# Kernel optimization log

Measured on AMD Instinct MI355X. Metric: run time of the kernel, lower is better.

The kernel has to match this reference:

```python
import jax, jax.numpy as jnp
import numpy as np

TRUNC = 2.0  # NSFP truncated chamfer: squared dists >= 2 are zeroed


def _mlp(x, W0, b0, Wh, bh, Wl, bl):
    h = jax.nn.relu(x @ W0 + b0)
    for i in range(Wh.shape[0]):
        h = jax.nn.relu(h @ Wh[i] + bh[i])
    return h @ Wl + bl


def _chamfer(x, y):
    d = (jnp.sum(x * x, axis=1)[:, None]
         + jnp.sum(y * y, axis=1)[None, :]
         - 2.0 * (x @ y.T))
    dx = jnp.min(d, axis=1)  # [N] NN dist x->y
    dy = jnp.min(d, axis=0)  # [M] NN dist y->x
    dx = jnp.where(dx < TRUNC, dx, 0.0)
    dy = jnp.where(dy < TRUNC, dy, 0.0)
    return jnp.mean(dx) + jnp.mean(dy)


def setup_inputs() -> dict:
    key = jax.random.key(0)
    ks = jax.random.split(key, 16)
    N = 20000
    F = 128
    H = 7  # hidden 128->128 layers (layer_size=8)
    s_in = 1.0 / np.sqrt(3.0)
    s_h = 1.0 / np.sqrt(F)
    d = {
        'pc0': jax.random.normal(ks[0], (N, 3), jnp.float32) * 10.0,
        'pc1': jax.random.normal(ks[1], (N, 3), jnp.float32) * 10.0,
        'W0': jax.random.normal(ks[2], (3, F), jnp.float32) * s_in,
        'b0': jnp.zeros((F,), jnp.float32),
        'Wh': jax.random.normal(ks[3], (H, F, F), jnp.float32) * s_h,
        'bh': jnp.zeros((H, F), jnp.float32),
        'Wl': jax.random.normal(ks[4], (F, 3), jnp.float32) * s_h,
        'bl': jnp.zeros((3,), jnp.float32),
        'W0i': jax.random.normal(ks[5], (3, F), jnp.float32) * s_in,
        'b0i': jnp.zeros((F,), jnp.float32),
        'Whi': jax.random.normal(ks[6], (H, F, F), jnp.float32) * s_h,
        'bhi': jnp.zeros((H, F), jnp.float32),
        'Wli': jax.random.normal(ks[7], (F, 3), jnp.float32) * s_h,
        'bli': jnp.zeros((3,), jnp.float32),
    }
    return d


def reference(pc0, pc1, W0, b0, Wh, bh, Wl, bl,
              W0i, b0i, Whi, bhi, Wli, bli):
    forward_flow = _mlp(pc0, W0, b0, Wh, bh, Wl, bl)          # [N,3]
    pc0_to_pc1 = pc0 + forward_flow
    inverse_flow = _mlp(pc0_to_pc1, W0i, b0i, Whi, bhi, Wli, bli)
    est_pc1_to_pc0 = pc0_to_pc1 - inverse_flow
    forward_loss = _chamfer(pc0_to_pc1, pc1)
    inverse_loss = _chamfer(est_pc1_to_pc0, pc0)
    return forward_loss + inverse_loss


if __name__ == '__main__':
    out = reference(**setup_inputs())
    print(out)
```

## Files before the change

### kernel.cpp

```cpp
#include <hip/hip_runtime.h>
#include <hip/hip_bf16.h>

#define F 128
#define NHID 7
#define BP 80
#define NPT 5
#define TRUNC_ 2.0f

#define GM 32
#define GM3 (GM * GM * GM)
#define GLO (-28.0f)
#define CELL 1.75f
#define GINV (1.0f / 1.75f)
#define SCAN_BLKS (GM3 / 256)
#define NGRID 4
#define PACKB 112
#define ZCB 128
#define ZB (NGRID * GM3 / 256)
#define BQ 128

typedef __attribute__((ext_vector_type(8))) short short8v;
typedef __attribute__((ext_vector_type(4))) float f32x4;

__device__ inline unsigned short f2bf(float v)
{
    __hip_bfloat16 b = __float2bfloat16(v);
    return __builtin_bit_cast(unsigned short, b);
}
__device__ inline float bf2f(unsigned short u)
{
    unsigned int x = ((unsigned int)u) << 16;
    return __builtin_bit_cast(float, x);
}

__device__ inline int hsw(int row, int col)
{
    return row * 128 + ((((col >> 3) ^ (row & 7)) << 3) | (col & 7));
}

__device__ inline void barrier_nd()
{
    asm volatile("s_waitcnt lgkmcnt(0)" ::: "memory");
    __builtin_amdgcn_s_barrier();
}

__global__ __launch_bounds__(256) void prep_kernel(
    const float* __restrict__ Wh, const float* __restrict__ Whi,
    const float* __restrict__ Wl, const float* __restrict__ Wli,
    unsigned short* __restrict__ whp,
    float* __restrict__ wlt, int* __restrict__ counts, unsigned int* __restrict__ done)
{
    int bid = blockIdx.x;
    int t = threadIdx.x;
    if (bid < PACKB) {
        int g = bid * 256 + t;
        int l = g & 63;
        int tt = (g >> 6) & 7;
        int s = (g >> 9) & 3;
        int m = g >> 11;
        int k0 = s * 32 + (l >> 4) * 8;
        int c = tt * 16 + (l & 15);
        const float* W = (m < 7 ? Wh + (size_t)m * F * F
                                : Whi + (size_t)(m - 7) * F * F);
        short8v v;
#pragma unroll
        for (int j = 0; j < 8; ++j)
            v[j] = (short)f2bf(W[(k0 + j) * F + c]);
        *(short8v*)(whp + (size_t)g * 8) = v;
    } else if (bid < PACKB + ZCB) {
        *(int4*)&counts[((bid - PACKB) * 256 + t) * 4] = make_int4(0, 0, 0, 0);
    } else {
#pragma unroll
        for (int r = 0; r < 3; ++r) {
            int e = r * 256 + t;
            int mI = e / 384;
            int rem = e - mI * 384;
            int c = rem >> 7;
            int k = rem & 127;
            const float* W = mI ? Wli : Wl;
            wlt[e] = W[k * 3 + c];
        }
        if (t == 0) *done = 0u;
    }
}

__device__ inline int cell_of(float x, float y, float z)
{
    int cx = (int)floorf((x - GLO) * GINV);
    int cy = (int)floorf((y - GLO) * GINV);
    int cz = (int)floorf((z - GLO) * GINV);
    cx = min(max(cx, 0), GM - 1);
    cy = min(max(cy, 0), GM - 1);
    cz = min(max(cz, 0), GM - 1);
    return (cz * GM + cy) * GM + cx;
}

__global__ __launch_bounds__(512, 2) void mlp_fused_kernel(
    const float* __restrict__ pc0, const float* __restrict__ pc1,
    const float* __restrict__ W0a, const float* __restrict__ b0a,
    const float* __restrict__ W0b, const float* __restrict__ b0b,
    const unsigned short* __restrict__ whp,
    const float* __restrict__ bha, const float* __restrict__ bhb,
    const float* __restrict__ wlt,
    const float* __restrict__ bla, const float* __restrict__ blb,
    float* __restrict__ Aout, float* __restrict__ Cout,
    int* __restrict__ counts, int N)
{
    __shared__ unsigned short hX[BP * 128];
    __shared__ unsigned short hY[BP * 128];
    __shared__ float Al[BP][4];
    __shared__ float Cl[BP][4];

    const int tid = threadIdx.x;
    const int lane = tid & 63;
    const int wv = tid >> 6;
    const int arow = lane & 15;
    const int kg = lane >> 4;
    const int p0 = blockIdx.x * BP;

    unsigned short* cur = hX;
    unsigned short* nxt = hY;

    short8v wA, wB;
    short8v hA[NPT], hB[NPT];

#define LW(WD, LI, S) { \
        size_t off = ((size_t)(((LI) * 4 + (S)) * 8 + wv) * 64 + lane) * 8; \
        WD = *(const short8v*)(whp + off); }
#define LH(D, S) { _Pragma("unroll") for (int p = 0; p < NPT; ++p) \
        D[p] = *(const short8v*)&cur[hsw(p * 16 + arow, (S) * 32 + kg * 8)]; }
#define MM(WD, H) { \
    _Pragma("unroll") for (int p = 0; p < NPT; ++p) \
        acc[p] = __builtin_amdgcn_mfma_f32_16x16x32_bf16(WD, H[p], acc[p], 0, 0, 0); }

    LW(wA, 0, 0)
    LW(wB, 0, 1)
    __builtin_amdgcn_sched_barrier(0);

    for (int M = 0; M < 2; ++M) {
        const float* W0 = M ? W0b : W0a;
        const float* b0 = M ? b0b : b0a;
        const float* bh = M ? bhb : bha;
        const float* bl = M ? blb : bla;

        {
            const int jg = tid & 31;
            const int pgg = tid >> 5;
            const int j0 = jg * 4;
            float4 wr0 = *(const float4*)(W0 + 0 * F + j0);
            float4 wr1 = *(const float4*)(W0 + 1 * F + j0);
            float4 wr2 = *(const float4*)(W0 + 2 * F + j0);
            float4 bb0 = *(const float4*)(b0 + j0);
#pragma unroll
            for (int p = 0; p < 5; ++p) {
                int pt = pgg * 5 + p;
                float x0, x1, x2;
                if (M == 0) {
                    int gp = p0 + pt;
                    int cp = gp < N ? gp : N - 1;
                    x0 = pc0[cp * 3 + 0]; x1 = pc0[cp * 3 + 1]; x2 = pc0[cp * 3 + 2];
                } else {
                    x0 = Al[pt][0]; x1 = Al[pt][1]; x2 = Al[pt][2];
                }
                float hx = fmaxf(fmaf(x0, wr0.x, fmaf(x1, wr1.x, fmaf(x2, wr2.x, bb0.x))), 0.f);
                float hy = fmaxf(fmaf(x0, wr0.y, fmaf(x1, wr1.y, fmaf(x2, wr2.y, bb0.y))), 0.f);
                float hz = fmaxf(fmaf(x0, wr0.z, fmaf(x1, wr1.z, fmaf(x2, wr2.z, bb0.z))), 0.f);
                float hw = fmaxf(fmaf(x0, wr0.w, fmaf(x1, wr1.w, fmaf(x2, wr2.w, bb0.w))), 0.f);
                short4 hv = make_short4((short)f2bf(hx), (short)f2bf(hy),
                                        (short)f2bf(hz), (short)f2bf(hw));
                *(short4*)&cur[hsw(pt, j0)] = hv;
            }
        }
        barrier_nd();

        for (int l = 0; l < NHID; ++l) {
            const int L = M * 7 + l;
            const int Ln = (L + 1 < 14) ? (L + 1) : 13;
            f32x4 acc[NPT];
            {
                float4 b4 = *(const float4*)&bh[l * F + wv * 16 + kg * 4];
#pragma unroll
                for (int p = 0; p < NPT; ++p)
                    acc[p] = (f32x4){b4.x, b4.y, b4.z, b4.w};
            }

            LH(hA, 0) LH(hB, 1)
            __builtin_amdgcn_sched_barrier(0);
            MM(wA, hA)
            LW(wA, L, 2) LH(hA, 2)
            __builtin_amdgcn_sched_barrier(0);
            MM(wB, hB)
            LW(wB, L, 3) LH(hB, 3)
            __builtin_amdgcn_sched_barrier(0);
            MM(wA, hA)
            LW(wA, Ln, 0)
            __builtin_amdgcn_sched_barrier(0);
            MM(wB, hB)
            LW(wB, Ln, 1)

#pragma unroll
            for (int p = 0; p < NPT; ++p) {
                float v0 = fmaxf(acc[p][0], 0.f), v1 = fmaxf(acc[p][1], 0.f);
                float v2 = fmaxf(acc[p][2], 0.f), v3 = fmaxf(acc[p][3], 0.f);
                short4 hv = make_short4((short)f2bf(v0), (short)f2bf(v1),
                                        (short)f2bf(v2), (short)f2bf(v3));
                *(short4*)&nxt[hsw(p * 16 + arow, wv * 16 + kg * 4)] = hv;
            }
            barrier_nd();
            unsigned short* tsw = cur; cur = nxt; nxt = tsw;
        }

        if (tid < 240) {
            int pt = tid / 3;
            int c = tid - 3 * pt;
            const float* wl = wlt + M * 384 + c * 128;
            float a0 = 0.f, a1 = 0.f, a2 = 0.f, a3 = 0.f;
#pragma unroll
            for (int q = 0; q < 16; ++q) {
                short8v h8 = *(const short8v*)&cur[hsw(pt, q * 8)];
                float4 wa = *(const float4*)(wl + q * 8);
                float4 wb = *(const float4*)(wl + q * 8 + 4);
                a0 = fmaf(bf2f((unsigned short)h8[0]), wa.x, a0);
                a1 = fmaf(bf2f((unsigned short)h8[1]), wa.y, a1);
                a2 = fmaf(bf2f((unsigned short)h8[2]), wa.z, a2);
                a3 = fmaf(bf2f((unsigned short)h8[3]), wa.w, a3);
                a0 = fmaf(bf2f((unsigned short)h8[4]), wb.x, a0);
                a1 = fmaf(bf2f((unsigned short)h8[5]), wb.y, a1);
                a2 = fmaf(bf2f((unsigned short)h8[6]), wb.z, a2);
                a3 = fmaf(bf2f((unsigned short)h8[7]), wb.w, a3);
            }
            float flow = ((a0 + a1) + (a2 + a3)) + bl[c];
            int gp = p0 + pt;
            int cp = gp < N ? gp : N - 1;
            if (M == 0) {
                float val = pc0[cp * 3 + c] + flow;
                Al[pt][c] = val;
                if (gp < N) Aout[gp * 3 + c] = val;
            } else {
                float val = Al[pt][c] - flow;
                Cl[pt][c] = val;
                if (gp < N) Cout[gp * 3 + c] = val;
            }
        }
        barrier_nd();
    }
#undef LW
#undef LH
#undef MM

    if (tid < BP) {
        int gp = p0 + tid;
        if (gp < N) {
            atomicAdd(&counts[1 * GM3 + cell_of(Al[tid][0], Al[tid][1], Al[tid][2])], 1);
            atomicAdd(&counts[3 * GM3 + cell_of(Cl[tid][0], Cl[tid][1], Cl[tid][2])], 1);
            atomicAdd(&counts[0 * GM3 + cell_of(pc1[gp * 3 + 0], pc1[gp * 3 + 1], pc1[gp * 3 + 2])], 1);
            atomicAdd(&counts[2 * GM3 + cell_of(pc0[gp * 3 + 0], pc0[gp * 3 + 1], pc0[gp * 3 + 2])], 1);
        }
    }
}

__device__ inline const float* cloud_ptr(int g, const float* g0, const float* g1,
                                         const float* g2, const float* g3)
{
    return g == 0 ? g0 : (g == 1 ? g1 : (g == 2 ? g2 : g3));
}

__global__ __launch_bounds__(256) void scan1(
    const int* __restrict__ counts, int* __restrict__ offs, int* __restrict__ bsum)
{
    int tid = threadIdx.x;
    int i = blockIdx.x * 256 + tid;
    int v = counts[i];
    __shared__ int s[256];
    s[tid] = v;
    __syncthreads();
#pragma unroll
    for (int off = 1; off < 256; off <<= 1) {
        int t = (tid >= off) ? s[tid - off] : 0;
        __syncthreads();
        s[tid] += t;
        __syncthreads();
    }
    offs[i] = s[tid] - v;
    if (tid == 255) bsum[blockIdx.x] = s[255];
}

__global__ __launch_bounds__(256) void scan23(
    int* __restrict__ offs, const int* __restrict__ bsum, int* __restrict__ counts)
{
    int seg = blockIdx.x / SCAN_BLKS;
    int pos = blockIdx.x - seg * SCAN_BLKS;
    const int* bs = bsum + seg * SCAN_BLKS;
    int t = threadIdx.x;
    int v = (t < pos) ? bs[t] : 0;
    __shared__ int red[4];
#pragma unroll
    for (int o = 32; o > 0; o >>= 1) v += __shfl_down(v, o, 64);
    if ((t & 63) == 0) red[t >> 6] = v;
    __syncthreads();
    int prefix = red[0] + red[1] + red[2] + red[3];
    int i = blockIdx.x * 256 + t;
    offs[i] += prefix;
    counts[i] = 0;
}

__global__ __launch_bounds__(256) void grid_fill(
    const float* __restrict__ B, const float* __restrict__ A,
    const float* __restrict__ D, const float* __restrict__ C,
    const int* __restrict__ offs, int* __restrict__ counts,
    float4* __restrict__ pts, int n)
{
    int g = blockIdx.y;
    const float* P = cloud_ptr(g, B, A, D, C);
    int i = blockIdx.x * 256 + threadIdx.x;
    if (i < n) {
        float x = P[i * 3 + 0], y = P[i * 3 + 1], z = P[i * 3 + 2];
        int c = g * GM3 + cell_of(x, y, z);
        int slot = offs[c] + atomicAdd(&counts[c], 1);
        pts[(size_t)g * n + slot] = make_float4(x, y, z, 0.f);
    }
}

__device__ inline float block_sum256(float v)
{
    __shared__ float sws[4];
#pragma unroll
    for (int o = 32; o > 0; o >>= 1) v += __shfl_down(v, o, 64);
    int w = threadIdx.x >> 6;
    if ((threadIdx.x & 63) == 0) sws[w] = v;
    __syncthreads();
    if (threadIdx.x == 0) v = sws[0] + sws[1] + sws[2] + sws[3];
    return v;
}

__device__ inline float boxd1(float q, int c)
{
    float lo = GLO + c * CELL;
    return fmaxf(fmaxf(lo - q, q - (lo + CELL)), 0.f);
}

__global__ __launch_bounds__(256) void grid_search(
    const int* __restrict__ offs, const int* __restrict__ counts,
    const float4* __restrict__ pts, float* __restrict__ partials,
    unsigned int* __restrict__ done, float* __restrict__ out, float inv, int n)
{
    const int d = blockIdx.y;
    const float4* Qs = pts + (size_t)(d ^ 1) * n;
    const float4* P  = pts + (size_t)d * n;
    const int* ofs = offs + (size_t)d * GM3;
    const int* cnt = counts + (size_t)d * GM3;

    const int tid = threadIdx.x;
    const int ql = tid & (BQ - 1);
    const int half = tid >> 7;
    const int i = blockIdx.x * BQ + ql;

    float mn = 3.4e38f;
    if (i < n) {
        float4 q = Qs[i];
        int cx = min(max((int)floorf((q.x - GLO) * GINV), 0), GM - 1);
        int cy = min(max((int)floorf((q.y - GLO) * GINV), 0), GM - 1);
        int cz = min(max((int)floorf((q.z - GLO) * GINV), 0), GM - 1);
        int xcl = max(cx - 1, 0), xch = min(cx + 1, GM - 1);
        int r0 = half * 4;

        int o[5], e[5];
#pragma unroll
        for (int r = 0; r < 5; ++r) {
            o[r] = 0; e[r] = 0;
            bool act = half ? true : (r < 4);
            if (act) {
                int rr = r0 + r;
                int dz = rr / 3, dy = rr - dz * 3;
                int z = cz + dz - 1;
                int y = cy + dy - 1;
                if ((unsigned)z < GM && (unsigned)y < GM) {
                    float dzd = boxd1(q.z, z);
                    float dyd = boxd1(q.y, y);
                    float dyz2 = fmaf(dzd, dzd, dyd * dyd);
                    if (dyz2 < TRUNC_) {
                        float rx = sqrtf(TRUNC_ - dyz2);
                        int xlo = max((int)floorf((q.x - rx - GLO) * GINV), xcl);
                        int xhi = min((int)floorf((q.x + rx - GLO) * GINV), xch);
                        if (xlo <= xhi) {
                            int rowbase = (z * GM + y) * GM;
                            o[r] = ofs[rowbase + xlo];
                            e[r] = ofs[rowbase + xhi] + cnt[rowbase + xhi];
                        }
                    }
                }
            }
        }
#pragma unroll
        for (int r = 0; r < 5; ++r) {
            for (int k = o[r]; k < e[r]; ++k) {
                float4 p = P[k];
                float ddx = q.x - p.x, ddy = q.y - p.y, ddz = q.z - p.z;
                mn = fminf(mn, fmaf(ddx, ddx, fmaf(ddy, ddy, ddz * ddz)));
            }
        }
    }

    __shared__ float m0[BQ];
    if (half == 0) m0[ql] = mn;
    __syncthreads();
    float val = 0.f;
    if (half == 1 && i < n) {
        float m = fminf(mn, m0[ql]);
        val = (m < TRUNC_) ? m : 0.f;
    }
    float bs = block_sum256(val);

    __shared__ int lastflag;
    if (tid == 0) {
        atomicExch(&partials[(size_t)d * gridDim.x + blockIdx.x], bs);
        __threadfence();
        unsigned v = atomicAdd(done, 1u);
        lastflag = (v == (unsigned)(NGRID * gridDim.x - 1)) ? 1 : 0;
    }
    __syncthreads();
    if (lastflag) {
        int NPt = NGRID * gridDim.x;
        float s = 0.f;
        for (int j = tid; j < NPt; j += 256)
            s += atomicAdd(&partials[j], 0.0f);
        __syncthreads();
        float tot = block_sum256(s);
        if (tid == 0) out[0] = tot * inv;
    }
}

extern "C" void kernel_launch(void* const* d_in, const int* in_sizes, int n_in,
                              void* d_out, int out_size, void* d_ws, size_t ws_size,
                              hipStream_t stream)
{
    const float* pc0 = (const float*)d_in[0];
    const float* pc1 = (const float*)d_in[1];
    const float* W0  = (const float*)d_in[2];
    const float* b0  = (const float*)d_in[3];
    const float* Wh  = (const float*)d_in[4];
    const float* bh  = (const float*)d_in[5];
    const float* Wl  = (const float*)d_in[6];
    const float* bl  = (const float*)d_in[7];
    const float* W0i = (const float*)d_in[8];
    const float* b0i = (const float*)d_in[9];
    const float* Whi = (const float*)d_in[10];
    const float* bhi = (const float*)d_in[11];
    const float* Wli = (const float*)d_in[12];
    const float* bli = (const float*)d_in[13];
    float* out = (float*)d_out;

    const int N = in_sizes[0] / 3;

    char* base = (char*)d_ws;
    float*  A        = (float*)(base + 0);
    float*  C        = (float*)(base + 240000);
    int*    counts   = (int*)  (base + 480000);
    int*    offs     = (int*)  (base + 1004288);
    int*    bsum     = (int*)  (base + 1528576);
    float4* pts      = (float4*)(base + 1532672);
    float*  partials = (float*)(base + 2812672);
    unsigned int* done = (unsigned int*)(base + 2816768);
    unsigned short* whp = (unsigned short*)(base + 2816784);
    float*  wlt      = (float*)(base + 3275536);

    const int PB = (N + 255) / 256;
    const int QB = (N + BQ - 1) / BQ;

    hipLaunchKernelGGL(prep_kernel, dim3(PACKB + ZCB + 1), dim3(256), 0, stream,
                       Wh, Whi, Wl, Wli, whp, wlt, counts, done);

    int mlpg = (N + BP - 1) / BP;
    hipLaunchKernelGGL(mlp_fused_kernel, dim3(mlpg), dim3(512), 0, stream,
                       pc0, pc1, W0, b0, W0i, b0i, whp, bh, bhi,
                       wlt, bl, bli, A, C, counts, N);

    hipLaunchKernelGGL(scan1, dim3(ZB), dim3(256), 0, stream, counts, offs, bsum);
    hipLaunchKernelGGL(scan23, dim3(ZB), dim3(256), 0, stream, offs, bsum, counts);
    hipLaunchKernelGGL(grid_fill, dim3(PB, NGRID), dim3(256), 0, stream,
                       pc1, A, pc0, C, offs, counts, pts, N);

    hipLaunchKernelGGL(grid_search, dim3(QB, NGRID), dim3(256), 0, stream,
                       offs, counts, pts, partials, done, out,
                       1.0f / (float)N, N);
}
```

Before: 76.67 us.

## Split MLP MFMA work across waves by point and feature groups

Each of the 8 waves previously owned 16 output features for all 80 points, so it loaded one weight fragment and all five point tiles from LDS per k-step. Now waves form a 2x4 grid: two point groups (3 or 2 tiles) by four feature groups (32 features each). Each wave loads two weight fragments and fewer LDS activation tiles, which cuts LDS reads. The cost is more weight loads per wave from global memory or cache, plus an uneven 3/2 point split that leaves some waves with less work.

```diff
diff --git a/kernel.cpp b/kernel.cpp
--- a/kernel.cpp
+++ b/kernel.cpp
@@ -4,7 +4,6 @@
 #define F 128
 #define NHID 7
 #define BP 80
-#define NPT 5
 #define TRUNC_ 2.0f
 
 #define GM 32
@@ -114,6 +113,10 @@
     const int tid = threadIdx.x;
     const int lane = tid & 63;
     const int wv = tid >> 6;
+    const int pg = wv & 1;
+    const int fg = wv >> 1;
+    const int pbase = pg * 3;
+    const int npt = pg ? 2 : 3;
     const int arow = lane & 15;
     const int kg = lane >> 4;
     const int p0 = blockIdx.x * BP;
@@ -121,20 +124,22 @@
     unsigned short* cur = hX;
     unsigned short* nxt = hY;
 
-    short8v wA, wB;
-    short8v hA[NPT], hB[NPT];
-
-#define LW(WD, LI, S) { \
-        size_t off = ((size_t)(((LI) * 4 + (S)) * 8 + wv) * 64 + lane) * 8; \
-        WD = *(const short8v*)(whp + off); }
-#define LH(D, S) { _Pragma("unroll") for (int p = 0; p < NPT; ++p) \
-        D[p] = *(const short8v*)&cur[hsw(p * 16 + arow, (S) * 32 + kg * 8)]; }
-#define MM(WD, H) { \
-    _Pragma("unroll") for (int p = 0; p < NPT; ++p) \
-        acc[p] = __builtin_amdgcn_mfma_f32_16x16x32_bf16(WD, H[p], acc[p], 0, 0, 0); }
-
-    LW(wA, 0, 0)
-    LW(wB, 0, 1)
+    short8v wA0, wA1, wB0, wB1;
+    short8v hA[3], hB[3];
+
+#define LW(WD0, WD1, LI, S) { \
+        size_t off = ((size_t)(((LI) * 4 + (S)) * 8 + fg * 2) * 64 + lane) * 8; \
+        WD0 = *(const short8v*)(whp + off); \
+        WD1 = *(const short8v*)(whp + off + 512); }
+#define LH(D, S) { _Pragma("unroll") for (int p = 0; p < 3; ++p) if (p < npt) \
+        D[p] = *(const short8v*)&cur[hsw((pbase + p) * 16 + arow, (S) * 32 + kg * 8)]; }
+#define MM(WD0, WD1, H) { \
+    _Pragma("unroll") for (int p = 0; p < 3; ++p) if (p < npt) { \
+        acc[p][0] = __builtin_amdgcn_mfma_f32_16x16x32_bf16(WD0, H[p], acc[p][0], 0, 0, 0); \
+        acc[p][1] = __builtin_amdgcn_mfma_f32_16x16x32_bf16(WD1, H[p], acc[p][1], 0, 0, 0); } }
+
+    LW(wA0, wA1, 0, 0)
+    LW(wB0, wB1, 0, 1)
     __builtin_amdgcn_sched_barrier(0);
 
     for (int M = 0; M < 2; ++M) {
@@ -176,35 +181,43 @@
         for (int l = 0; l < NHID; ++l) {
             const int L = M * 7 + l;
             const int Ln = (L + 1 < 14) ? (L + 1) : 13;
-            f32x4 acc[NPT];
-            {
-                float4 b4 = *(const float4*)&bh[l * F + wv * 16 + kg * 4];
-#pragma unroll
-                for (int p = 0; p < NPT; ++p)
-                    acc[p] = (f32x4){b4.x, b4.y, b4.z, b4.w};
+            f32x4 acc[3][2];
+#pragma unroll
+            for (int p = 0; p < 3; ++p) {
+#pragma unroll
+                for (int m = 0; m < 2; ++m) {
+                    float4 b4 = *(const float4*)&bh[l * F + (fg * 2 + m) * 16 + kg * 4];
+                    acc[p][m] = (f32x4){b4.x, b4.y, b4.z, b4.w};
+                }
             }
 
             LH(hA, 0) LH(hB, 1)
             __builtin_amdgcn_sched_barrier(0);
-            MM(wA, hA)
-            LW(wA, L, 2) LH(hA, 2)
+            MM(wA0, wA1, hA)
+            LW(wA0, wA1, L, 2) LH(hA, 2)
             __builtin_amdgcn_sched_barrier(0);
-            MM(wB, hB)
-            LW(wB, L, 3) LH(hB, 3)
+            MM(wB0, wB1, hB)
+            LW(wB0, wB1, L, 3) LH(hB, 3)
             __builtin_amdgcn_sched_barrier(0);
-            MM(wA, hA)
-            LW(wA, Ln, 0)
+            MM(wA0, wA1, hA)
+            LW(wA0, wA1, Ln, 0)
             __builtin_amdgcn_sched_barrier(0);
-            MM(wB, hB)
-            LW(wB, Ln, 1)
-
-#pragma unroll
-            for (int p = 0; p < NPT; ++p) {
-                float v0 = fmaxf(acc[p][0], 0.f), v1 = fmaxf(acc[p][1], 0.f);
-                float v2 = fmaxf(acc[p][2], 0.f), v3 = fmaxf(acc[p][3], 0.f);
-                short4 hv = make_short4((short)f2bf(v0), (short)f2bf(v1),
-                                        (short)f2bf(v2), (short)f2bf(v3));
-                *(short4*)&nxt[hsw(p * 16 + arow, wv * 16 + kg * 4)] = hv;
+            MM(wB0, wB1, hB)
+            LW(wB0, wB1, Ln, 1)
+
+#pragma unroll
+            for (int p = 0; p < 3; ++p) {
+                if (p < npt) {
+#pragma unroll
+                    for (int m = 0; m < 2; ++m) {
+                        float v0 = fmaxf(acc[p][m][0], 0.f), v1 = fmaxf(acc[p][m][1], 0.f);
+                        float v2 = fmaxf(acc[p][m][2], 0.f), v3 = fmaxf(acc[p][m][3], 0.f);
+                        short4 hv = make_short4((short)f2bf(v0), (short)f2bf(v1),
+                                                (short)f2bf(v2), (short)f2bf(v3));
+                        *(short4*)&nxt[hsw((pbase + p) * 16 + arow,
+                                           (fg * 2 + m) * 16 + kg * 4)] = hv;
+                    }
+                }
             }
             barrier_nd();
             unsigned short* tsw = cur; cur = nxt; nxt = tsw;
```

New measurement: 78.19 us. About the same (+2.0%).

## Compute both chamfer directions from one search pass using atomicMin on targets

Applied to the files above, without the earlier changes.

Grid search now runs over two directions instead of four. Each query-to-target distance below the truncation is also pushed into a per-target atomicMin buffer, which supplies the reverse nearest-neighbour distance. The buffer is initialised in the prep kernel, and the last block sums it serially in the final reduction. This halves the neighbour search work, but adds many global atomics in the inner loop and a serial 2N-element reduction in a single block.

```diff
diff --git a/kernel.cpp b/kernel.cpp
--- a/kernel.cpp
+++ b/kernel.cpp
@@ -14,8 +14,10 @@
 #define GINV (1.0f / 1.75f)
 #define SCAN_BLKS (GM3 / 256)
 #define NGRID 4
+#define NDIR 2
 #define PACKB 112
 #define ZCB 128
+#define QMB 40
 #define ZB (NGRID * GM3 / 256)
 #define BQ 128
 
@@ -48,7 +50,8 @@
     const float* __restrict__ Wh, const float* __restrict__ Whi,
     const float* __restrict__ Wl, const float* __restrict__ Wli,
     unsigned short* __restrict__ whp,
-    float* __restrict__ wlt, int* __restrict__ counts, unsigned int* __restrict__ done)
+    float* __restrict__ wlt, int* __restrict__ counts,
+    unsigned int* __restrict__ done, unsigned int* __restrict__ qmins)
 {
     int bid = blockIdx.x;
     int t = threadIdx.x;
@@ -69,7 +72,7 @@
         *(short8v*)(whp + (size_t)g * 8) = v;
     } else if (bid < PACKB + ZCB) {
         *(int4*)&counts[((bid - PACKB) * 256 + t) * 4] = make_int4(0, 0, 0, 0);
-    } else {
+    } else if (bid == PACKB + ZCB) {
 #pragma unroll
         for (int r = 0; r < 3; ++r) {
             int e = r * 256 + t;
@@ -81,6 +84,10 @@
             wlt[e] = W[k * 3 + c];
         }
         if (t == 0) *done = 0u;
+    } else {
+        const unsigned int inf = 0x7f7fffffu;
+        uint4 v = make_uint4(inf, inf, inf, inf);
+        *(uint4*)&qmins[((bid - PACKB - ZCB - 1) * 256 + t) * 4] = v;
     }
 }
 
@@ -342,13 +349,16 @@
 __global__ __launch_bounds__(256) void grid_search(
     const int* __restrict__ offs, const int* __restrict__ counts,
     const float4* __restrict__ pts, float* __restrict__ partials,
+    unsigned int* __restrict__ qmins,
     unsigned int* __restrict__ done, float* __restrict__ out, float inv, int n)
 {
     const int d = blockIdx.y;
-    const float4* Qs = pts + (size_t)(d ^ 1) * n;
-    const float4* P  = pts + (size_t)d * n;
-    const int* ofs = offs + (size_t)d * GM3;
-    const int* cnt = counts + (size_t)d * GM3;
+    const int gq = 2 * d + 1, gt = 2 * d;
+    const float4* Qs = pts + (size_t)gq * n;
+    const float4* P  = pts + (size_t)gt * n;
+    const int* ofs = offs + (size_t)gt * GM3;
+    const int* cnt = counts + (size_t)gt * GM3;
+    unsigned int* qm = qmins + (size_t)d * n;
 
     const int tid = threadIdx.x;
     const int ql = tid & (BQ - 1);
@@ -396,7 +406,10 @@
             for (int k = o[r]; k < e[r]; ++k) {
                 float4 p = P[k];
                 float ddx = q.x - p.x, ddy = q.y - p.y, ddz = q.z - p.z;
-                mn = fminf(mn, fmaf(ddx, ddx, fmaf(ddy, ddy, ddz * ddz)));
+                float dd = fmaf(ddx, ddx, fmaf(ddy, ddy, ddz * ddz));
+                mn = fminf(mn, dd);
+                if (dd < TRUNC_)
+                    atomicMin(&qm[k], __float_as_uint(dd));
             }
         }
     }
@@ -416,14 +429,19 @@
         atomicExch(&partials[(size_t)d * gridDim.x + blockIdx.x], bs);
         __threadfence();
         unsigned v = atomicAdd(done, 1u);
-        lastflag = (v == (unsigned)(NGRID * gridDim.x - 1)) ? 1 : 0;
+        lastflag = (v == (unsigned)(NDIR * gridDim.x - 1)) ? 1 : 0;
     }
     __syncthreads();
     if (lastflag) {
-        int NPt = NGRID * gridDim.x;
+        int NPt = NDIR * gridDim.x;
         float s = 0.f;
         for (int j = tid; j < NPt; j += 256)
             s += atomicAdd(&partials[j], 0.0f);
+        for (int j = tid; j < 2 * n; j += 256) {
+            unsigned u = atomicAdd(&qmins[j], 0u);
+            float m = __uint_as_float(u);
+            s += (m < TRUNC_) ? m : 0.f;
+        }
         __syncthreads();
         float tot = block_sum256(s);
         if (tid == 0) out[0] = tot * inv;
@@ -463,12 +481,13 @@
     unsigned int* done = (unsigned int*)(base + 2816768);
     unsigned short* whp = (unsigned short*)(base + 2816784);
     float*  wlt      = (float*)(base + 3275536);
+    unsigned int* qmins = (unsigned int*)(base + 3278608);
 
     const int PB = (N + 255) / 256;
     const int QB = (N + BQ - 1) / BQ;
 
-    hipLaunchKernelGGL(prep_kernel, dim3(PACKB + ZCB + 1), dim3(256), 0, stream,
-                       Wh, Whi, Wl, Wli, whp, wlt, counts, done);
+    hipLaunchKernelGGL(prep_kernel, dim3(PACKB + ZCB + 1 + QMB), dim3(256), 0, stream,
+                       Wh, Whi, Wl, Wli, whp, wlt, counts, done, qmins);
 
     int mlpg = (N + BP - 1) / BP;
     hipLaunchKernelGGL(mlp_fused_kernel, dim3(mlpg), dim3(512), 0, stream,
@@ -480,7 +499,7 @@
     hipLaunchKernelGGL(grid_fill, dim3(PB, NGRID), dim3(256), 0, stream,
                        pc1, A, pc0, C, offs, counts, pts, N);
 
-    hipLaunchKernelGGL(grid_search, dim3(QB, NGRID), dim3(256), 0, stream,
-                       offs, counts, pts, partials, done, out,
+    hipLaunchKernelGGL(grid_search, dim3(QB, NDIR), dim3(256), 0, stream,
+                       offs, counts, pts, partials, qmins, done, out,
                        1.0f / (float)N, N);
 }
```

Result: slower. 137.9 us (+79.9%).
